# Kernel tuning notes

Measured on AMD Instinct MI355X. Metric: run time of the kernel, lower is better.

## Reference

```python
import jax, jax.numpy as jnp
import numpy as np

EPS = 1e-08


def setup_inputs() -> dict:
    key = jax.random.key(0)
    B, C, T = 4, 512, 32000
    x = jax.random.normal(key, (B, C, T), dtype=jnp.float32)
    weight = jnp.ones((C,), dtype=jnp.float32)
    bias = jnp.zeros((C,), dtype=jnp.float32)
    return {"x": x, "weight": weight, "bias": bias}


def reference(x, weight, bias):
    # Cumulative LayerNorm over (C, 0..t) for each time step t, 3D input (B, C, T).
    # Note: sum_C(cumsum_T(x)) == cumsum_T(sum_C(x)); reduce channels first (cheaper, same math).
    B, C, T = x.shape
    step = jnp.arange(1, T + 1, dtype=x.dtype)            # (T,)
    count = (step * C)[None, None, :]                     # (1,1,T)
    cum_sum = jnp.cumsum(x.sum(axis=1, keepdims=True), axis=-1)          # (B,1,T)
    cum_sum_sq = jnp.cumsum((x * x).sum(axis=1, keepdims=True), axis=-1)  # (B,1,T)
    cum_mean = cum_sum / count
    cum_var = jnp.maximum(cum_sum_sq / count - cum_mean * cum_mean, 0.0)
    y = (x - cum_mean) / jnp.sqrt(cum_var + EPS)
    return y * weight[None, :, None] + bias[None, :, None]
```

## Files before the change

### kernel.cpp

```cpp
#include <hip/hip_runtime.h>
#include <math.h>

#define EPS 1e-8

constexpr int W = 32;
constexpr int W4 = W / 4;
constexpr int NTHR = 512;
constexpr int CMAX = 512;

struct __align__(16) dbl2 {
  double s, q;
};

__global__ __launch_bounds__(NTHR, 4) void clnorm_reduce(
    const float4* __restrict__ x4, dbl2* __restrict__ scanBuf,
    dbl2* __restrict__ aggBuf, int B, int C, int T, int nCh) {
  const int T4 = T >> 2;
  const int ch = blockIdx.x;
  const int b = blockIdx.y;
  const int tid = threadIdx.x;
  const int t0 = ch * W;
  const int t40 = t0 >> 2;

  const int p = tid >> 3;
  const int t4 = tid & (W4 - 1);
  const int cPer = C / 64;

  float4 s4 = make_float4(0.f, 0.f, 0.f, 0.f);
  float4 q4 = make_float4(0.f, 0.f, 0.f, 0.f);
  if (t40 + t4 < T4) {
    const float4* xp = x4 + ((size_t)b * C + (size_t)p * cPer) * T4 + t40 + t4;
#pragma unroll
    for (int k = 0; k < cPer; ++k) {
      float4 v = xp[(size_t)k * T4];
      s4.x += v.x;
      s4.y += v.y;
      s4.z += v.z;
      s4.w += v.w;
      q4.x = fmaf(v.x, v.x, q4.x);
      q4.y = fmaf(v.y, v.y, q4.y);
      q4.z = fmaf(v.z, v.z, q4.z);
      q4.w = fmaf(v.w, v.w, q4.w);
    }
  }
  __shared__ float4 ps_sh[64 * W4];
  __shared__ float4 pq_sh[64 * W4];
  ps_sh[p * W4 + t4] = s4;
  pq_sh[p * W4 + t4] = q4;
  __syncthreads();

  if (tid < 64) {
    const int lane = tid;
    double as = 0.0, aq = 0.0;
    if (lane < W) {
      const float* psf = (const float*)ps_sh;
      const float* pqf = (const float*)pq_sh;
#pragma unroll 8
      for (int pp = 0; pp < 64; ++pp) {
        as += (double)psf[pp * W + lane];
        aq += (double)pqf[pp * W + lane];
      }
    }
    for (int off = 1; off < W; off <<= 1) {
      double vs = __shfl_up(as, off, 64);
      double vq = __shfl_up(aq, off, 64);
      if (lane >= off && lane < W) {
        as += vs;
        aq += vq;
      }
    }
    if (lane < W && t0 + lane < T)
      scanBuf[(size_t)b * T + t0 + lane] = dbl2{as, aq};
    if (lane == W - 1) aggBuf[(size_t)b * nCh + ch] = dbl2{as, aq};
  }
}

__global__ __launch_bounds__(NTHR, 4) void clnorm_apply(
    const float4* __restrict__ x4, const float* __restrict__ wgt,
    const float* __restrict__ bias, const dbl2* __restrict__ scanBuf,
    const dbl2* __restrict__ aggBuf, float4* __restrict__ y4, int B, int C,
    int T, int nCh) {
  const int T4 = T >> 2;
  const int ch = blockIdx.x;
  const int b = blockIdx.y;
  const int tid = threadIdx.x;
  const int t0 = ch * W;
  const int t40 = t0 >> 2;

  __shared__ float w_sh[CMAX];
  __shared__ float b_sh[CMAX];
  __shared__ __align__(16) float m_sh[W];
  __shared__ __align__(16) float r_sh[W];

  const int c0 = tid >> 3;
  const int t4 = tid & (W4 - 1);
  const bool inb = (t40 + t4 < T4);

  float4 xv[8];
  const float4* xp = x4 + ((size_t)b * C + c0) * T4 + t40 + t4;
  if (inb) {
#pragma unroll
    for (int j = 0; j < 8; ++j) xv[j] = xp[(size_t)(j * 64) * T4];
  }
  for (int c = tid; c < C; c += NTHR) {
    w_sh[c] = wgt[c];
    b_sh[c] = bias[c];
  }

  if (tid < 64) {
    const int lane = tid;
    double es = 0.0, eq = 0.0;
    const dbl2* ag = aggBuf + (size_t)b * nCh;
    for (int base = 0; base < ch; base += 64) {
      int i = base + lane;
      if (i < ch) {
        dbl2 a = ag[i];
        es += a.s;
        eq += a.q;
      }
    }
#pragma unroll
    for (int o = 32; o > 0; o >>= 1) {
      es += __shfl_xor(es, o, 64);
      eq += __shfl_xor(eq, o, 64);
    }
    if (lane < W && t0 + lane < T) {
      dbl2 pp = scanBuf[(size_t)b * T + t0 + lane];
      double cnt = (double)(t0 + lane + 1) * (double)C;
      double m = (es + pp.s) / cnt;
      double var = (eq + pp.q) / cnt - m * m;
      if (var < 0.0) var = 0.0;
      m_sh[lane] = (float)m;
      r_sh[lane] = (float)(1.0 / sqrt(var + EPS));
    }
  }
  __syncthreads();

  if (inb) {
    float4 mv = *(const float4*)&m_sh[t4 * 4];
    float4 rv = *(const float4*)&r_sh[t4 * 4];
    float4* yp = y4 + ((size_t)b * C + c0) * T4 + t40 + t4;
#pragma unroll
    for (int j = 0; j < 8; ++j) {
      int c = c0 + j * 64;
      float wc = w_sh[c], bc = b_sh[c];
      float4 yv;
      yv.x = (xv[j].x - mv.x) * rv.x * wc + bc;
      yv.y = (xv[j].y - mv.y) * rv.y * wc + bc;
      yv.z = (xv[j].z - mv.z) * rv.z * wc + bc;
      yv.w = (xv[j].w - mv.w) * rv.w * wc + bc;
      yp[(size_t)(j * 64) * T4] = yv;
    }
  }
}

extern "C" void kernel_launch(void* const* d_in, const int* in_sizes, int n_in,
                              void* d_out, int out_size, void* d_ws,
                              size_t ws_size, hipStream_t stream) {
  const float4* x4 = (const float4*)d_in[0];
  const float* w = (const float*)d_in[1];
  const float* bias = (const float*)d_in[2];
  float4* y4 = (float4*)d_out;

  int B = 4;
  int C = in_sizes[1];
  int T = in_sizes[0] / (B * C);
  int nCh = (T + W - 1) / W;

  dbl2* scanBuf = (dbl2*)d_ws;
  dbl2* aggBuf = scanBuf + (size_t)B * T;

  dim3 g(nCh, B);
  clnorm_reduce<<<g, NTHR, 0, stream>>>(x4, scanBuf, aggBuf, B, C, T, nCh);
  clnorm_apply<<<g, NTHR, 0, stream>>>(x4, w, bias, scanBuf, aggBuf, y4, B, C,
                                       T, nCh);
}
```

Before: 514.4 us.

## Replace per-block prefix aggregation with dedicated chunk-offset scan kernel

```diff
diff --git a/kernel.cpp b/kernel.cpp
--- a/kernel.cpp
+++ b/kernel.cpp
@@ -5,16 +5,13 @@
 
 constexpr int W = 32;
 constexpr int W4 = W / 4;
-constexpr int NTHR = 512;
+constexpr int NTHR = 256;
 constexpr int CMAX = 512;
 
-struct __align__(16) dbl2 {
-  double s, q;
-};
-
 __global__ __launch_bounds__(NTHR, 4) void clnorm_reduce(
-    const float4* __restrict__ x4, dbl2* __restrict__ scanBuf,
-    dbl2* __restrict__ aggBuf, int B, int C, int T, int nCh) {
+    const float4* __restrict__ x4, double* __restrict__ scanS,
+    double* __restrict__ scanQ, double* __restrict__ aggS,
+    double* __restrict__ aggQ, int B, int C, int T, int nCh) {
   const int T4 = T >> 2;
   const int ch = blockIdx.x;
   const int b = blockIdx.y;
@@ -24,13 +21,13 @@
 
   const int p = tid >> 3;
   const int t4 = tid & (W4 - 1);
-  const int cPer = C / 64;
+  const int cPer = C / 32;
 
   float4 s4 = make_float4(0.f, 0.f, 0.f, 0.f);
   float4 q4 = make_float4(0.f, 0.f, 0.f, 0.f);
   if (t40 + t4 < T4) {
     const float4* xp = x4 + ((size_t)b * C + (size_t)p * cPer) * T4 + t40 + t4;
-#pragma unroll
+#pragma unroll 4
     for (int k = 0; k < cPer; ++k) {
       float4 v = xp[(size_t)k * T4];
       s4.x += v.x;
@@ -43,42 +40,77 @@
       q4.w = fmaf(v.w, v.w, q4.w);
     }
   }
-  __shared__ float4 ps_sh[64 * W4];
-  __shared__ float4 pq_sh[64 * W4];
-  ps_sh[p * W4 + t4] = s4;
-  pq_sh[p * W4 + t4] = q4;
+  __shared__ float4 ps4[32 * W4];
+  __shared__ float4 pq4[32 * W4];
+  ps4[p * W4 + t4] = s4;
+  pq4[p * W4 + t4] = q4;
   __syncthreads();
 
-  if (tid < 64) {
-    const int lane = tid;
-    double as = 0.0, aq = 0.0;
-    if (lane < W) {
-      const float* psf = (const float*)ps_sh;
-      const float* pqf = (const float*)pq_sh;
+  const int wave = tid >> 6;
+  const int lane = tid & 63;
+  if (wave < 2 && lane < W) {
+    const float* src = (wave == 0) ? (const float*)ps4 : (const float*)pq4;
+    double a = 0.0;
 #pragma unroll 8
-      for (int pp = 0; pp < 64; ++pp) {
-        as += (double)psf[pp * W + lane];
-        aq += (double)pqf[pp * W + lane];
-      }
+    for (int pp = 0; pp < 32; ++pp)
+      a += (double)src[pp * W + lane];
+    for (int off = 1; off < W; off <<= 1) {
+      double v = __shfl_up(a, off, 64);
+      if (lane >= off) a += v;
     }
-    for (int off = 1; off < W; off <<= 1) {
-      double vs = __shfl_up(as, off, 64);
-      double vq = __shfl_up(aq, off, 64);
-      if (lane >= off && lane < W) {
-        as += vs;
-        aq += vq;
-      }
+    if (t0 + lane < T) {
+      double* dst = (wave == 0) ? scanS : scanQ;
+      dst[(size_t)b * T + t0 + lane] = a;
     }
-    if (lane < W && t0 + lane < T)
-      scanBuf[(size_t)b * T + t0 + lane] = dbl2{as, aq};
-    if (lane == W - 1) aggBuf[(size_t)b * nCh + ch] = dbl2{as, aq};
+    if (lane == W - 1) {
+      double* ad = (wave == 0) ? aggS : aggQ;
+      ad[(size_t)b * nCh + ch] = a;
+    }
+  }
+}
+
+__global__ __launch_bounds__(512) void clnorm_scanagg(
+    const double* __restrict__ aggS, const double* __restrict__ aggQ,
+    double* __restrict__ offS, double* __restrict__ offQ, int nCh) {
+  const int b = blockIdx.x;
+  const int tid = threadIdx.x;
+  __shared__ double shS[512];
+  __shared__ double shQ[512];
+
+  const int i0 = tid * 2, i1 = tid * 2 + 1;
+  const size_t base = (size_t)b * nCh;
+  double s0 = (i0 < nCh) ? aggS[base + i0] : 0.0;
+  double s1 = (i1 < nCh) ? aggS[base + i1] : 0.0;
+  double q0 = (i0 < nCh) ? aggQ[base + i0] : 0.0;
+  double q1 = (i1 < nCh) ? aggQ[base + i1] : 0.0;
+  shS[tid] = s0 + s1;
+  shQ[tid] = q0 + q1;
+  __syncthreads();
+  for (int off = 1; off < 512; off <<= 1) {
+    double vs = (tid >= off) ? shS[tid - off] : 0.0;
+    double vq = (tid >= off) ? shQ[tid - off] : 0.0;
+    __syncthreads();
+    shS[tid] += vs;
+    shQ[tid] += vq;
+    __syncthreads();
+  }
+  double exS = shS[tid] - (s0 + s1);
+  double exQ = shQ[tid] - (q0 + q1);
+  if (i0 < nCh) {
+    offS[base + i0] = exS;
+    offQ[base + i0] = exQ;
+  }
+  if (i1 < nCh) {
+    offS[base + i1] = exS + s0;
+    offQ[base + i1] = exQ + q0;
   }
 }
 
 __global__ __launch_bounds__(NTHR, 4) void clnorm_apply(
     const float4* __restrict__ x4, const float* __restrict__ wgt,
-    const float* __restrict__ bias, const dbl2* __restrict__ scanBuf,
-    const dbl2* __restrict__ aggBuf, float4* __restrict__ y4, int B, int C,
+    const float* __restrict__ bias, const double* __restrict__ scanS,
+    const double* __restrict__ scanQ, const double* __restrict__ offS,
+    const double* __restrict__ offQ, float4* __restrict__ y4, int B, int C,
     int T, int nCh) {
   const int T4 = T >> 2;
   const int ch = blockIdx.x;
@@ -92,65 +124,41 @@
   __shared__ __align__(16) float m_sh[W];
   __shared__ __align__(16) float r_sh[W];
 
-  const int c0 = tid >> 3;
-  const int t4 = tid & (W4 - 1);
-  const bool inb = (t40 + t4 < T4);
-
-  float4 xv[8];
-  const float4* xp = x4 + ((size_t)b * C + c0) * T4 + t40 + t4;
-  if (inb) {
-#pragma unroll
-    for (int j = 0; j < 8; ++j) xv[j] = xp[(size_t)(j * 64) * T4];
-  }
   for (int c = tid; c < C; c += NTHR) {
     w_sh[c] = wgt[c];
     b_sh[c] = bias[c];
   }
 
-  if (tid < 64) {
-    const int lane = tid;
-    double es = 0.0, eq = 0.0;
-    const dbl2* ag = aggBuf + (size_t)b * nCh;
-    for (int base = 0; base < ch; base += 64) {
-      int i = base + lane;
-      if (i < ch) {
-        dbl2 a = ag[i];
-        es += a.s;
-        eq += a.q;
-      }
-    }
-#pragma unroll
-    for (int o = 32; o > 0; o >>= 1) {
-      es += __shfl_xor(es, o, 64);
-      eq += __shfl_xor(eq, o, 64);
-    }
-    if (lane < W && t0 + lane < T) {
-      dbl2 pp = scanBuf[(size_t)b * T + t0 + lane];
-      double cnt = (double)(t0 + lane + 1) * (double)C;
-      double m = (es + pp.s) / cnt;
-      double var = (eq + pp.q) / cnt - m * m;
-      if (var < 0.0) var = 0.0;
-      m_sh[lane] = (float)m;
-      r_sh[lane] = (float)(1.0 / sqrt(var + EPS));
-    }
+  if (tid < W && t0 + tid < T) {
+    double s = offS[(size_t)b * nCh + ch] + scanS[(size_t)b * T + t0 + tid];
+    double q = offQ[(size_t)b * nCh + ch] + scanQ[(size_t)b * T + t0 + tid];
+    double cnt = (double)(t0 + tid + 1) * (double)C;
+    double m = s / cnt;
+    double var = q / cnt - m * m;
+    if (var < 0.0) var = 0.0;
+    m_sh[tid] = (float)m;
+    r_sh[tid] = (float)(1.0 / sqrt(var + EPS));
   }
   __syncthreads();
 
-  if (inb) {
-    float4 mv = *(const float4*)&m_sh[t4 * 4];
-    float4 rv = *(const float4*)&r_sh[t4 * 4];
-    float4* yp = y4 + ((size_t)b * C + c0) * T4 + t40 + t4;
-#pragma unroll
-    for (int j = 0; j < 8; ++j) {
-      int c = c0 + j * 64;
-      float wc = w_sh[c], bc = b_sh[c];
-      float4 yv;
-      yv.x = (xv[j].x - mv.x) * rv.x * wc + bc;
-      yv.y = (xv[j].y - mv.y) * rv.y * wc + bc;
-      yv.z = (xv[j].z - mv.z) * rv.z * wc + bc;
-      yv.w = (xv[j].w - mv.w) * rv.w * wc + bc;
-      yp[(size_t)(j * 64) * T4] = yv;
-    }
+  const int c0 = tid >> 3;
+  const int t4 = tid & (W4 - 1);
+  if (t40 + t4 >= T4) return;
+  const float4 mv = *(const float4*)&m_sh[t4 * 4];
+  const float4 rv = *(const float4*)&r_sh[t4 * 4];
+  const float4* xp = x4 + ((size_t)b * C + c0) * T4 + t40 + t4;
+  float4* yp = y4 + ((size_t)b * C + c0) * T4 + t40 + t4;
+#pragma unroll 4
+  for (int j = 0; j < CMAX / 32; ++j) {
+    int c = c0 + j * 32;
+    float4 xv = xp[(size_t)(j * 32) * T4];
+    float wc = w_sh[c], bc = b_sh[c];
+    float4 yv;
+    yv.x = (xv.x - mv.x) * rv.x * wc + bc;
+    yv.y = (xv.y - mv.y) * rv.y * wc + bc;
+    yv.z = (xv.z - mv.z) * rv.z * wc + bc;
+    yv.w = (xv.w - mv.w) * rv.w * wc + bc;
+    yp[(size_t)(j * 32) * T4] = yv;
   }
 }
 
@@ -167,11 +175,17 @@
   int T = in_sizes[0] / (B * C);
   int nCh = (T + W - 1) / W;
 
-  dbl2* scanBuf = (dbl2*)d_ws;
-  dbl2* aggBuf = scanBuf + (size_t)B * T;
+  double* scanS = (double*)d_ws;
+  double* scanQ = scanS + (size_t)B * T;
+  double* aggS = scanQ + (size_t)B * T;
+  double* aggQ = aggS + (size_t)B * nCh;
+  double* offS = aggQ + (size_t)B * nCh;
+  double* offQ = offS + (size_t)B * nCh;
 
   dim3 g(nCh, B);
-  clnorm_reduce<<<g, NTHR, 0, stream>>>(x4, scanBuf, aggBuf, B, C, T, nCh);
-  clnorm_apply<<<g, NTHR, 0, stream>>>(x4, w, bias, scanBuf, aggBuf, y4, B, C,
-                                       T, nCh);
+  clnorm_reduce<<<g, NTHR, 0, stream>>>(x4, scanS, scanQ, aggS, aggQ, B, C, T,
+                                        nCh);
+  clnorm_scanagg<<<dim3(B), 512, 0, stream>>>(aggS, aggQ, offS, offQ, nCh);
+  clnorm_apply<<<g, NTHR, 0, stream>>>(x4, w, bias, scanS, scanQ, offS, offQ,
+                                       y4, B, C, T, nCh);
 }
```

After: 512.8 us. No clear change (-0.3%).
